# Optimization experiments

Measured on AMD Instinct MI355X. Metric: run time of the kernel, lower is better.

## Reference

```python
import jax, jax.numpy as jnp
import numpy as np

B, C, H, W = 4, 64, 64, 64
CQ = C // 8

def setup_inputs() -> dict:
    key = jax.random.key(0)
    ks = jax.random.split(key, 8)
    s = 1.0 / np.sqrt(C)
    return {
        "x": jax.random.normal(ks[0], (B, C, H, W), dtype=jnp.float32),
        "Wq": jax.random.normal(ks[1], (CQ, C), dtype=jnp.float32) * s,
        "bq": jax.random.normal(ks[2], (CQ,), dtype=jnp.float32) * 0.01,
        "Wk": jax.random.normal(ks[3], (CQ, C), dtype=jnp.float32) * s,
        "bk": jax.random.normal(ks[4], (CQ,), dtype=jnp.float32) * 0.01,
        "Wv": jax.random.normal(ks[5], (C, C), dtype=jnp.float32) * s,
        "bv": jax.random.normal(ks[6], (C,), dtype=jnp.float32) * 0.01,
        "gamma": jax.random.normal(ks[7], (1,), dtype=jnp.float32) * 0.1,
    }

def reference(x, Wq, bq, Wk, bk, Wv, bv, gamma):
    b, c, h, w = x.shape
    n = h * w
    xf = x.reshape(b, c, n)  # [B, C, N]
    # 1x1 convs are pointwise channel projections
    q = jnp.einsum('oc,bcn->bon', Wq, xf) + bq[None, :, None]  # [B, CQ, N]
    k = jnp.einsum('oc,bcn->bon', Wk, xf) + bk[None, :, None]  # [B, CQ, N]
    v = jnp.einsum('oc,bcn->bon', Wv, xf) + bv[None, :, None]  # [B, C, N]
    energy = jnp.einsum('bcn,bcm->bnm', q, k)                  # [B, N, N]
    attn = jax.nn.softmax(energy, axis=-1)
    out = jnp.einsum('bcm,bnm->bcn', v, attn)                  # [B, C, N]
    out = out.reshape(b, c, h, w)
    return gamma[0] * out + x
```

## Files before the change

### kernel.cpp

```cpp
#include <hip/hip_runtime.h>
#include <hip/hip_bf16.h>


typedef __attribute__((ext_vector_type(8))) short short8;
typedef __attribute__((ext_vector_type(4))) float f32x4;
typedef __attribute__((ext_vector_type(4))) unsigned uint4v;
typedef unsigned short ushort_t;

#define NSEQ 4096
#define LOG2E 1.4426950408889634f

__device__ __forceinline__ unsigned pk_bf16(float lo, float hi) {
  const unsigned short a = __builtin_bit_cast(unsigned short, __float2bfloat16(lo));
  const unsigned short b = __builtin_bit_cast(unsigned short, __float2bfloat16(hi));
  return (unsigned)a | ((unsigned)b << 16);
}

__global__ __launch_bounds__(256, 4) void proj_kernel(
    const float* __restrict__ x,
    const float* __restrict__ Wq, const float* __restrict__ bq,
    const float* __restrict__ Wk, const float* __restrict__ bk,
    const float* __restrict__ Wv, const float* __restrict__ bv,
    ushort_t* __restrict__ Qb, ushort_t* __restrict__ Kb,
    ushort_t* __restrict__ Vb)
{
  const int tid  = threadIdx.x;
  const int lane = tid & 63;
  const int w    = __builtin_amdgcn_readfirstlane(tid >> 6);
  const int blk  = blockIdx.x;
  const int quarter = blk & 3;
  const int g    = (blk >> 2) & 63;
  const int b    = blk >> 8;
  const int n    = g * 64 + lane;

  const float* xb = x + (size_t)(b * 64) * NSEQ + n;
  const int co0 = quarter * 16 + w * 4;
  const float* w0 = Wv + (co0 + 0) * 64;
  const float* w1 = Wv + (co0 + 1) * 64;
  const float* w2 = Wv + (co0 + 2) * 64;
  const float* w3 = Wv + (co0 + 3) * 64;
  const int p = quarter * 4 + w;
  const float* wr = (p < 8) ? (Wq + p * 64) : (Wk + (p - 8) * 64);
  float a0 = bv[co0 + 0], a1 = bv[co0 + 1], a2 = bv[co0 + 2], a3 = bv[co0 + 3];
  float aq = (p < 8) ? bq[p] : bk[p - 8];

#pragma unroll
  for (int kc = 0; kc < 64; kc += 8) {
    float xv[8];
#pragma unroll
    for (int i = 0; i < 8; ++i) xv[i] = xb[(size_t)(kc + i) * NSEQ];
#pragma unroll
    for (int i = 0; i < 8; ++i) {
      const float xk = xv[i];
      a0 += w0[kc + i] * xk;
      a1 += w1[kc + i] * xk;
      a2 += w2[kc + i] * xk;
      a3 += w3[kc + i] * xk;
      aq += wr[kc + i] * xk;
    }
  }

  ushort_t* vt = Vb + ((size_t)(b * 128 + (n >> 5)) * 64 + co0) * 32 + (n & 31);
  vt[0]  = __builtin_bit_cast(ushort_t, __float2bfloat16(a0));
  vt[32] = __builtin_bit_cast(ushort_t, __float2bfloat16(a1));
  vt[64] = __builtin_bit_cast(ushort_t, __float2bfloat16(a2));
  vt[96] = __builtin_bit_cast(ushort_t, __float2bfloat16(a3));

  if (p < 8) aq *= LOG2E;
  ushort_t* qk = ((p < 8) ? Qb : Kb) + ((size_t)(b * NSEQ + n)) * 8 + (p & 7);
  *qk = __builtin_bit_cast(ushort_t, __float2bfloat16(aq));
}

__global__ __launch_bounds__(512, 4) void attn_kernel(
    const ushort_t* __restrict__ Qb, const ushort_t* __restrict__ Kb,
    const ushort_t* __restrict__ Vb, const float* __restrict__ x,
    const float* __restrict__ gamma, float* __restrict__ out)
{
  __shared__ float buf[4][64][36];

  const int tid  = threadIdx.x;
  const int wave = __builtin_amdgcn_readfirstlane(tid >> 6);
  const int lane = tid & 63;
  const int q16  = lane & 15;
  const int quad = lane >> 4;
  const int blk  = blockIdx.x;
  const int b    = blk >> 7;
  const int n0   = (blk & 127) << 5;
  const int mbase = wave << 9;

  const short8 z8 = {0, 0, 0, 0, 0, 0, 0, 0};
  short8 qfA = *(const short8*)(Qb + ((size_t)(b * NSEQ + n0 + q16)) * 8);
  short8 qfB = *(const short8*)(Qb + ((size_t)(b * NSEQ + n0 + 16 + q16)) * 8);
  if (quad != 0) { qfA = z8; qfB = z8; }

  const int mperm = 8 * (q16 >> 2) + (q16 & 3);
  const char* kbase = (const char*)(Kb + ((size_t)(b * NSEQ + mbase + mperm)) * 8);
  const char* vbase = (const char*)(Vb + ((size_t)(b * 128 + (mbase >> 5)) * 64) * 32)
                      + q16 * 64 + quad * 16;

  f32x4 aA0 = {0.f, 0.f, 0.f, 0.f};
  f32x4 aA1 = aA0, aA2 = aA0, aA3 = aA0;
  f32x4 aB0 = aA0, aB1 = aA0, aB2 = aA0, aB3 = aA0;
  float lA = 0.f, lB = 0.f;

#pragma unroll 2
  for (int t = 0; t < 16; ++t) {
    const char* kp = kbase + (size_t)t * 512;
    const char* vp = vbase + (size_t)t * 4096;
    const short8 kf0 = *(const short8*)(kp);
    const short8 kf1 = *(const short8*)(kp + 64);
    const short8 vf0 = *(const short8*)(vp);
    const short8 vf1 = *(const short8*)(vp + 1024);
    const short8 vf2 = *(const short8*)(vp + 2048);
    const short8 vf3 = *(const short8*)(vp + 3072);

    const f32x4 z = {0.f, 0.f, 0.f, 0.f};
    f32x4 s0 = __builtin_amdgcn_mfma_f32_16x16x32_bf16(kf0, qfA, z, 0, 0, 0);
    f32x4 s1 = __builtin_amdgcn_mfma_f32_16x16x32_bf16(kf1, qfA, z, 0, 0, 0);
    f32x4 s2 = __builtin_amdgcn_mfma_f32_16x16x32_bf16(kf0, qfB, z, 0, 0, 0);
    f32x4 s3 = __builtin_amdgcn_mfma_f32_16x16x32_bf16(kf1, qfB, z, 0, 0, 0);

    float pA0 = __builtin_amdgcn_exp2f(s0[0]);
    float pA1 = __builtin_amdgcn_exp2f(s0[1]);
    float pA2 = __builtin_amdgcn_exp2f(s0[2]);
    float pA3 = __builtin_amdgcn_exp2f(s0[3]);
    float pA4 = __builtin_amdgcn_exp2f(s1[0]);
    float pA5 = __builtin_amdgcn_exp2f(s1[1]);
    float pA6 = __builtin_amdgcn_exp2f(s1[2]);
    float pA7 = __builtin_amdgcn_exp2f(s1[3]);
    float pB0 = __builtin_amdgcn_exp2f(s2[0]);
    float pB1 = __builtin_amdgcn_exp2f(s2[1]);
    float pB2 = __builtin_amdgcn_exp2f(s2[2]);
    float pB3 = __builtin_amdgcn_exp2f(s2[3]);
    float pB4 = __builtin_amdgcn_exp2f(s3[0]);
    float pB5 = __builtin_amdgcn_exp2f(s3[1]);
    float pB6 = __builtin_amdgcn_exp2f(s3[2]);
    float pB7 = __builtin_amdgcn_exp2f(s3[3]);
    lA += ((pA0 + pA1) + (pA2 + pA3)) + ((pA4 + pA5) + (pA6 + pA7));
    lB += ((pB0 + pB1) + (pB2 + pB3)) + ((pB4 + pB5) + (pB6 + pB7));

    const uint4v uA = {pk_bf16(pA0, pA1), pk_bf16(pA2, pA3),
                       pk_bf16(pA4, pA5), pk_bf16(pA6, pA7)};
    const uint4v uB = {pk_bf16(pB0, pB1), pk_bf16(pB2, pB3),
                       pk_bf16(pB4, pB5), pk_bf16(pB6, pB7)};
    const short8 pfA = __builtin_bit_cast(short8, uA);
    const short8 pfB = __builtin_bit_cast(short8, uB);

    aA0 = __builtin_amdgcn_mfma_f32_16x16x32_bf16(vf0, pfA, aA0, 0, 0, 0);
    aA1 = __builtin_amdgcn_mfma_f32_16x16x32_bf16(vf1, pfA, aA1, 0, 0, 0);
    aA2 = __builtin_amdgcn_mfma_f32_16x16x32_bf16(vf2, pfA, aA2, 0, 0, 0);
    aA3 = __builtin_amdgcn_mfma_f32_16x16x32_bf16(vf3, pfA, aA3, 0, 0, 0);
    aB0 = __builtin_amdgcn_mfma_f32_16x16x32_bf16(vf0, pfB, aB0, 0, 0, 0);
    aB1 = __builtin_amdgcn_mfma_f32_16x16x32_bf16(vf1, pfB, aB1, 0, 0, 0);
    aB2 = __builtin_amdgcn_mfma_f32_16x16x32_bf16(vf2, pfB, aB2, 0, 0, 0);
    aB3 = __builtin_amdgcn_mfma_f32_16x16x32_bf16(vf3, pfB, aB3, 0, 0, 0);
  }

  lA += __shfl_xor(lA, 16); lA += __shfl_xor(lA, 32);
  lB += __shfl_xor(lB, 16); lB += __shfl_xor(lB, 32);

  f32x4 aAs[4] = {aA0, aA1, aA2, aA3};
  f32x4 aBs[4] = {aB0, aB1, aB2, aB3};

  if (wave >= 4) {
    float* d = &buf[wave - 4][lane][0];
#pragma unroll
    for (int j = 0; j < 4; ++j)
#pragma unroll
      for (int r = 0; r < 4; ++r) {
        d[j * 4 + r]      = aAs[j][r];
        d[16 + j * 4 + r] = aBs[j][r];
      }
    d[32] = lA; d[33] = lB;
  }
  __syncthreads();
  if (wave < 4) {
    float* d = &buf[wave][lane][0];
#pragma unroll
    for (int j = 0; j < 4; ++j)
#pragma unroll
      for (int r = 0; r < 4; ++r) {
        aAs[j][r] += d[j * 4 + r];
        aBs[j][r] += d[16 + j * 4 + r];
      }
    lA += d[32]; lB += d[33];
#pragma unroll
    for (int j = 0; j < 4; ++j)
#pragma unroll
      for (int r = 0; r < 4; ++r) {
        d[j * 4 + r]      = aAs[j][r];
        d[16 + j * 4 + r] = aBs[j][r];
      }
    d[32] = lA; d[33] = lB;
  }
  __syncthreads();

  const int qt = wave >> 2;
  const int cg = wave & 3;
  float fr[4] = {0.f, 0.f, 0.f, 0.f};
  float lt = 0.f;
#pragma unroll
  for (int w2 = 0; w2 < 4; ++w2) {
    lt += buf[w2][lane][32 + qt];
#pragma unroll
    for (int r = 0; r < 4; ++r) fr[r] += buf[w2][lane][qt * 16 + cg * 4 + r];
  }

  const float ginv = gamma[0] / lt;
  const int nn = n0 + qt * 16 + q16;
#pragma unroll
  for (int r = 0; r < 4; ++r) {
    const int c = cg * 16 + quad * 4 + r;
    const size_t idx = ((size_t)(b * 64 + c)) * NSEQ + nn;
    out[idx] = fr[r] * ginv + x[idx];
  }
}

extern "C" void kernel_launch(void* const* d_in, const int* in_sizes, int n_in,
                              void* d_out, int out_size, void* d_ws, size_t ws_size,
                              hipStream_t stream) {
  (void)in_sizes; (void)n_in; (void)out_size; (void)ws_size;
  const float* x     = (const float*)d_in[0];
  const float* Wq    = (const float*)d_in[1];
  const float* bq    = (const float*)d_in[2];
  const float* Wk    = (const float*)d_in[3];
  const float* bk    = (const float*)d_in[4];
  const float* Wv    = (const float*)d_in[5];
  const float* bv    = (const float*)d_in[6];
  const float* gamma = (const float*)d_in[7];
  float* out = (float*)d_out;

  ushort_t* Qb = (ushort_t*)d_ws;
  ushort_t* Kb = (ushort_t*)((char*)d_ws + (256u << 10));
  ushort_t* Vb = (ushort_t*)((char*)d_ws + (512u << 10));

  hipLaunchKernelGGL(proj_kernel, dim3(1024), dim3(256), 0, stream,
                     x, Wq, bq, Wk, bk, Wv, bv, Qb, Kb, Vb);
  hipLaunchKernelGGL(attn_kernel, dim3(512), dim3(512), 0, stream,
                     Qb, Kb, Vb, x, gamma, out);
}
```

Baseline: 96.10 us.

## Process 64 queries per attention block to reuse K/V fragments across four query tiles

Each attention block now handles 64 query rows instead of 32, so every K and V fragment loaded per iteration feeds four query tiles instead of two. This halves the grid to 256 blocks and halves total K/V global traffic. In exchange it doubles the accumulator registers, lowers launch bounds occupancy to 2, grows the shared reduction buffer, and leaves only 256 blocks for the 256 CUs, which reduces latency hiding.

```diff
diff --git a/kernel.cpp b/kernel.cpp
--- a/kernel.cpp
+++ b/kernel.cpp
@@ -71,12 +71,12 @@
   *qk = __builtin_bit_cast(ushort_t, __float2bfloat16(aq));
 }
 
-__global__ __launch_bounds__(512, 4) void attn_kernel(
+__global__ __launch_bounds__(512, 2) void attn_kernel(
     const ushort_t* __restrict__ Qb, const ushort_t* __restrict__ Kb,
     const ushort_t* __restrict__ Vb, const float* __restrict__ x,
     const float* __restrict__ gamma, float* __restrict__ out)
 {
-  __shared__ float buf[4][64][36];
+  __shared__ float buf[4][64][69];
 
   const int tid  = threadIdx.x;
   const int wave = __builtin_amdgcn_readfirstlane(tid >> 6);
@@ -84,26 +84,31 @@
   const int q16  = lane & 15;
   const int quad = lane >> 4;
   const int blk  = blockIdx.x;
-  const int b    = blk >> 7;
-  const int n0   = (blk & 127) << 5;
+  const int b    = blk >> 6;
+  const int n0   = (blk & 63) << 6;
   const int mbase = wave << 9;
 
   const short8 z8 = {0, 0, 0, 0, 0, 0, 0, 0};
-  short8 qfA = *(const short8*)(Qb + ((size_t)(b * NSEQ + n0 + q16)) * 8);
-  short8 qfB = *(const short8*)(Qb + ((size_t)(b * NSEQ + n0 + 16 + q16)) * 8);
-  if (quad != 0) { qfA = z8; qfB = z8; }
+  short8 qf[4];
+#pragma unroll
+  for (int qt = 0; qt < 4; ++qt) {
+    qf[qt] = *(const short8*)(Qb + ((size_t)(b * NSEQ + n0 + qt * 16 + q16)) * 8);
+    if (quad != 0) qf[qt] = z8;
+  }
 
   const int mperm = 8 * (q16 >> 2) + (q16 & 3);
   const char* kbase = (const char*)(Kb + ((size_t)(b * NSEQ + mbase + mperm)) * 8);
   const char* vbase = (const char*)(Vb + ((size_t)(b * 128 + (mbase >> 5)) * 64) * 32)
                       + q16 * 64 + quad * 16;
 
-  f32x4 aA0 = {0.f, 0.f, 0.f, 0.f};
-  f32x4 aA1 = aA0, aA2 = aA0, aA3 = aA0;
-  f32x4 aB0 = aA0, aB1 = aA0, aB2 = aA0, aB3 = aA0;
-  float lA = 0.f, lB = 0.f;
-
-#pragma unroll 2
+  f32x4 acc[4][4];
+#pragma unroll
+  for (int qt = 0; qt < 4; ++qt)
+#pragma unroll
+    for (int cf = 0; cf < 4; ++cf) acc[qt][cf] = (f32x4){0.f, 0.f, 0.f, 0.f};
+  float l[4] = {0.f, 0.f, 0.f, 0.f};
+
+#pragma unroll 1
   for (int t = 0; t < 16; ++t) {
     const char* kp = kbase + (size_t)t * 512;
     const char* vp = vbase + (size_t)t * 4096;
@@ -114,105 +119,90 @@
     const short8 vf2 = *(const short8*)(vp + 2048);
     const short8 vf3 = *(const short8*)(vp + 3072);
 
-    const f32x4 z = {0.f, 0.f, 0.f, 0.f};
-    f32x4 s0 = __builtin_amdgcn_mfma_f32_16x16x32_bf16(kf0, qfA, z, 0, 0, 0);
-    f32x4 s1 = __builtin_amdgcn_mfma_f32_16x16x32_bf16(kf1, qfA, z, 0, 0, 0);
-    f32x4 s2 = __builtin_amdgcn_mfma_f32_16x16x32_bf16(kf0, qfB, z, 0, 0, 0);
-    f32x4 s3 = __builtin_amdgcn_mfma_f32_16x16x32_bf16(kf1, qfB, z, 0, 0, 0);
-
-    float pA0 = __builtin_amdgcn_exp2f(s0[0]);
-    float pA1 = __builtin_amdgcn_exp2f(s0[1]);
-    float pA2 = __builtin_amdgcn_exp2f(s0[2]);
-    float pA3 = __builtin_amdgcn_exp2f(s0[3]);
-    float pA4 = __builtin_amdgcn_exp2f(s1[0]);
-    float pA5 = __builtin_amdgcn_exp2f(s1[1]);
-    float pA6 = __builtin_amdgcn_exp2f(s1[2]);
-    float pA7 = __builtin_amdgcn_exp2f(s1[3]);
-    float pB0 = __builtin_amdgcn_exp2f(s2[0]);
-    float pB1 = __builtin_amdgcn_exp2f(s2[1]);
-    float pB2 = __builtin_amdgcn_exp2f(s2[2]);
-    float pB3 = __builtin_amdgcn_exp2f(s2[3]);
-    float pB4 = __builtin_amdgcn_exp2f(s3[0]);
-    float pB5 = __builtin_amdgcn_exp2f(s3[1]);
-    float pB6 = __builtin_amdgcn_exp2f(s3[2]);
-    float pB7 = __builtin_amdgcn_exp2f(s3[3]);
-    lA += ((pA0 + pA1) + (pA2 + pA3)) + ((pA4 + pA5) + (pA6 + pA7));
-    lB += ((pB0 + pB1) + (pB2 + pB3)) + ((pB4 + pB5) + (pB6 + pB7));
-
-    const uint4v uA = {pk_bf16(pA0, pA1), pk_bf16(pA2, pA3),
-                       pk_bf16(pA4, pA5), pk_bf16(pA6, pA7)};
-    const uint4v uB = {pk_bf16(pB0, pB1), pk_bf16(pB2, pB3),
-                       pk_bf16(pB4, pB5), pk_bf16(pB6, pB7)};
-    const short8 pfA = __builtin_bit_cast(short8, uA);
-    const short8 pfB = __builtin_bit_cast(short8, uB);
-
-    aA0 = __builtin_amdgcn_mfma_f32_16x16x32_bf16(vf0, pfA, aA0, 0, 0, 0);
-    aA1 = __builtin_amdgcn_mfma_f32_16x16x32_bf16(vf1, pfA, aA1, 0, 0, 0);
-    aA2 = __builtin_amdgcn_mfma_f32_16x16x32_bf16(vf2, pfA, aA2, 0, 0, 0);
-    aA3 = __builtin_amdgcn_mfma_f32_16x16x32_bf16(vf3, pfA, aA3, 0, 0, 0);
-    aB0 = __builtin_amdgcn_mfma_f32_16x16x32_bf16(vf0, pfB, aB0, 0, 0, 0);
-    aB1 = __builtin_amdgcn_mfma_f32_16x16x32_bf16(vf1, pfB, aB1, 0, 0, 0);
-    aB2 = __builtin_amdgcn_mfma_f32_16x16x32_bf16(vf2, pfB, aB2, 0, 0, 0);
-    aB3 = __builtin_amdgcn_mfma_f32_16x16x32_bf16(vf3, pfB, aB3, 0, 0, 0);
-  }
-
-  lA += __shfl_xor(lA, 16); lA += __shfl_xor(lA, 32);
-  lB += __shfl_xor(lB, 16); lB += __shfl_xor(lB, 32);
-
-  f32x4 aAs[4] = {aA0, aA1, aA2, aA3};
-  f32x4 aBs[4] = {aB0, aB1, aB2, aB3};
+#pragma unroll
+    for (int qt = 0; qt < 4; ++qt) {
+      const f32x4 z = {0.f, 0.f, 0.f, 0.f};
+      f32x4 s0 = __builtin_amdgcn_mfma_f32_16x16x32_bf16(kf0, qf[qt], z, 0, 0, 0);
+      f32x4 s1 = __builtin_amdgcn_mfma_f32_16x16x32_bf16(kf1, qf[qt], z, 0, 0, 0);
+
+      const float p0 = __builtin_amdgcn_exp2f(s0[0]);
+      const float p1 = __builtin_amdgcn_exp2f(s0[1]);
+      const float p2 = __builtin_amdgcn_exp2f(s0[2]);
+      const float p3 = __builtin_amdgcn_exp2f(s0[3]);
+      const float p4 = __builtin_amdgcn_exp2f(s1[0]);
+      const float p5 = __builtin_amdgcn_exp2f(s1[1]);
+      const float p6 = __builtin_amdgcn_exp2f(s1[2]);
+      const float p7 = __builtin_amdgcn_exp2f(s1[3]);
+      l[qt] += ((p0 + p1) + (p2 + p3)) + ((p4 + p5) + (p6 + p7));
+
+      const uint4v u = {pk_bf16(p0, p1), pk_bf16(p2, p3),
+                        pk_bf16(p4, p5), pk_bf16(p6, p7)};
+      const short8 pf = __builtin_bit_cast(short8, u);
+
+      acc[qt][0] = __builtin_amdgcn_mfma_f32_16x16x32_bf16(vf0, pf, acc[qt][0], 0, 0, 0);
+      acc[qt][1] = __builtin_amdgcn_mfma_f32_16x16x32_bf16(vf1, pf, acc[qt][1], 0, 0, 0);
+      acc[qt][2] = __builtin_amdgcn_mfma_f32_16x16x32_bf16(vf2, pf, acc[qt][2], 0, 0, 0);
+      acc[qt][3] = __builtin_amdgcn_mfma_f32_16x16x32_bf16(vf3, pf, acc[qt][3], 0, 0, 0);
+    }
+  }
+
+#pragma unroll
+  for (int qt = 0; qt < 4; ++qt) {
+    l[qt] += __shfl_xor(l[qt], 16);
+    l[qt] += __shfl_xor(l[qt], 32);
+  }
 
   if (wave >= 4) {
     float* d = &buf[wave - 4][lane][0];
 #pragma unroll
-    for (int j = 0; j < 4; ++j)
-#pragma unroll
-      for (int r = 0; r < 4; ++r) {
-        d[j * 4 + r]      = aAs[j][r];
-        d[16 + j * 4 + r] = aBs[j][r];
-      }
-    d[32] = lA; d[33] = lB;
+    for (int qt = 0; qt < 4; ++qt) {
+#pragma unroll
+      for (int cf = 0; cf < 4; ++cf)
+#pragma unroll
+        for (int r = 0; r < 4; ++r) d[qt * 16 + cf * 4 + r] = acc[qt][cf][r];
+      d[64 + qt] = l[qt];
+    }
   }
   __syncthreads();
   if (wave < 4) {
     float* d = &buf[wave][lane][0];
 #pragma unroll
-    for (int j = 0; j < 4; ++j)
-#pragma unroll
-      for (int r = 0; r < 4; ++r) {
-        aAs[j][r] += d[j * 4 + r];
-        aBs[j][r] += d[16 + j * 4 + r];
-      }
-    lA += d[32]; lB += d[33];
-#pragma unroll
-    for (int j = 0; j < 4; ++j)
-#pragma unroll
-      for (int r = 0; r < 4; ++r) {
-        d[j * 4 + r]      = aAs[j][r];
-        d[16 + j * 4 + r] = aBs[j][r];
-      }
-    d[32] = lA; d[33] = lB;
+    for (int qt = 0; qt < 4; ++qt) {
+#pragma unroll
+      for (int cf = 0; cf < 4; ++cf)
+#pragma unroll
+        for (int r = 0; r < 4; ++r) {
+          acc[qt][cf][r] += d[qt * 16 + cf * 4 + r];
+          d[qt * 16 + cf * 4 + r] = acc[qt][cf][r];
+        }
+      l[qt] += d[64 + qt];
+      d[64 + qt] = l[qt];
+    }
   }
   __syncthreads();
 
-  const int qt = wave >> 2;
-  const int cg = wave & 3;
-  float fr[4] = {0.f, 0.f, 0.f, 0.f};
+  const int qt = wave >> 1;
+  const int cg0 = (wave & 1) * 2;
   float lt = 0.f;
 #pragma unroll
-  for (int w2 = 0; w2 < 4; ++w2) {
-    lt += buf[w2][lane][32 + qt];
-#pragma unroll
-    for (int r = 0; r < 4; ++r) fr[r] += buf[w2][lane][qt * 16 + cg * 4 + r];
-  }
-
+  for (int w2 = 0; w2 < 4; ++w2) lt += buf[w2][lane][64 + qt];
   const float ginv = gamma[0] / lt;
   const int nn = n0 + qt * 16 + q16;
-#pragma unroll
-  for (int r = 0; r < 4; ++r) {
-    const int c = cg * 16 + quad * 4 + r;
-    const size_t idx = ((size_t)(b * 64 + c)) * NSEQ + nn;
-    out[idx] = fr[r] * ginv + x[idx];
+
+#pragma unroll
+  for (int h = 0; h < 2; ++h) {
+    const int cg = cg0 + h;
+    float fr[4] = {0.f, 0.f, 0.f, 0.f};
+#pragma unroll
+    for (int w2 = 0; w2 < 4; ++w2)
+#pragma unroll
+      for (int r = 0; r < 4; ++r) fr[r] += buf[w2][lane][qt * 16 + cg * 4 + r];
+#pragma unroll
+    for (int r = 0; r < 4; ++r) {
+      const int c = cg * 16 + quad * 4 + r;
+      const size_t idx = ((size_t)(b * 64 + c)) * NSEQ + nn;
+      out[idx] = fr[r] * ginv + x[idx];
+    }
   }
 }
 
@@ -236,6 +226,6 @@
 
   hipLaunchKernelGGL(proj_kernel, dim3(1024), dim3(256), 0, stream,
                      x, Wq, bq, Wk, bk, Wv, bv, Qb, Kb, Vb);
-  hipLaunchKernelGGL(attn_kernel, dim3(512), dim3(512), 0, stream,
+  hipLaunchKernelGGL(attn_kernel, dim3(256), dim3(512), 0, stream,
                      Qb, Kb, Vb, x, gamma, out);
 }
```

Result: no change. 95.22 us, median of 2 (-0.9%).
